# Performance work log

Measured on AMD Instinct MI355X. Metric: run time of the kernel, lower is better.

## Reference

```python
import jax, jax.numpy as jnp
import numpy as np

G = 131072            # number of graphs
NPG = 38              # nodes per graph (from reshape to (*, 38))
N = G * NPG           # total nodes
E = 10 * N            # total edges (avg degree 10)


def leaky_relu(x):
    return jnp.where(x >= 0, x, 0.01 * x)


def setup_inputs() -> dict:
    key = jax.random.key(0)
    ks = jax.random.split(key, 13)
    s = 0.1
    return {
        "x": jax.random.normal(ks[0], (N, 1), jnp.float32),
        "edge_index": jax.random.randint(ks[1], (2, E), 0, N, dtype=jnp.int64)
            if jax.config.read("jax_enable_x64") else jax.random.randint(ks[1], (2, E), 0, N, dtype=jnp.int32),
        "edge_attr": jax.random.normal(ks[2], (E, 1), jnp.float32),
        # NNConv(1,1, Linear(1,1)) params
        "w_edge": jax.random.normal(ks[3], (1, 1), jnp.float32) * s,  # edge MLP weight
        "b_edge": jax.random.normal(ks[4], (1,), jnp.float32) * s,   # edge MLP bias
        "w_root": jax.random.normal(ks[5], (1, 1), jnp.float32) * s, # NNConv root weight
        "b_conv": jax.random.normal(ks[6], (1,), jnp.float32) * s,   # NNConv bias
        # head MLP: 38 -> 4 -> 4 -> 12 (stored as (in, out))
        "W1": jax.random.normal(ks[7], (38, 4), jnp.float32) * s,
        "b1": jax.random.normal(ks[8], (4,), jnp.float32) * s,
        "W2": jax.random.normal(ks[9], (4, 4), jnp.float32) * s,
        "b2": jax.random.normal(ks[10], (4,), jnp.float32) * s,
        "W3": jax.random.normal(ks[11], (4, 12), jnp.float32) * s,
        "b3": jax.random.normal(ks[12], (12,), jnp.float32) * s,
    }


def reference(x, edge_index, edge_attr, w_edge, b_edge, w_root, b_conv,
              W1, b1, W2, b2, W3, b3):
    src, dst = edge_index[0], edge_index[1]
    # per-edge 1x1 transform produced by edge MLP: theta_e = Linear(edge_attr)
    theta = edge_attr @ w_edge + b_edge            # [E, 1]
    # message = x_src * theta (in=out=1 so the matmul is a scalar product)
    msg = x[src] * theta                           # [E, 1] gather + multiply
    agg = jax.ops.segment_sum(msg, dst, num_segments=N)  # scatter-add to targets
    nodes = agg + x @ w_root + b_conv              # [N, 1] add aggr + root + bias
    # dense head over per-graph node vectors (dropout is identity at eval)
    h = nodes.reshape(G, NPG)                      # [G, 38]
    h = leaky_relu(h @ W1 + b1)                    # [G, 4]
    h = leaky_relu(h @ W2 + b2)                    # [G, 4]
    h = leaky_relu(h @ W3 + b3)                    # [G, 12]
    return jax.nn.softmax(h, axis=-1)
```

## Files before the change

### kernel.cpp

```cpp
#include <hip/hip_runtime.h>
#include <hip/hip_fp16.h>

#define NPG 38
#define HEAD_BLK 256
#define SHIFT 14
#define SLICE (1 << SHIFT)
#define DBMAX 320
#define NSB 8
#define NB1 1024
#define P1_THR 512
#define CH 8192
#define P2_THR 512

typedef int      v4i __attribute__((ext_vector_type(4)));
typedef float    v4f __attribute__((ext_vector_type(4)));
typedef unsigned v2u __attribute__((ext_vector_type(2)));

static inline __device__ unsigned short f2h(float f) {
    return __half_as_ushort(__float2half(f));
}
static inline __device__ float h2f(unsigned short b) {
    return __half2float(__ushort_as_half(b));
}

__global__ __launch_bounds__(P1_THR) void k_p1a(
    const int* __restrict__ src, int nquads, int qpb, int sbsz,
    int* __restrict__ histM8)
{
    __shared__ int h8[NSB];
    const int tid = threadIdx.x;
    if (tid < NSB) h8[tid] = 0;
    __syncthreads();
    const int blk = blockIdx.x;
    const int q0 = blk * qpb;
    const int q1 = min(q0 + qpb, nquads);
    const v4i* s4 = (const v4i*)src;
    for (int q = q0 + tid; q < q1; q += P1_THR) {
        v4i s = __builtin_nontemporal_load(s4 + q);
        atomicAdd(&h8[s.x / sbsz], 1);
        atomicAdd(&h8[s.y / sbsz], 1);
        atomicAdd(&h8[s.z / sbsz], 1);
        atomicAdd(&h8[s.w / sbsz], 1);
    }
    __syncthreads();
    if (tid < NSB) histM8[tid * NB1 + blk] = h8[tid];
}

__global__ __launch_bounds__(512) void k_scanM(
    int* __restrict__ histM8, int* __restrict__ sseg)
{
    __shared__ int stot[NSB];
    __shared__ int sbase[NSB + 1];
    const int tid = threadIdx.x;
    const int wid = tid >> 6, lane = tid & 63;

    const int base = wid * NB1 + lane * (NB1 / 64);
    int vals[NB1 / 64];
    int s = 0;
    #pragma unroll
    for (int k = 0; k < NB1 / 64; ++k) { vals[k] = s; s += histM8[base + k]; }
    int excl = s;
    #pragma unroll
    for (int d = 1; d < 64; d <<= 1) {
        int t = __shfl_up(excl, d, 64);
        if (lane >= d) excl += t;
    }
    excl -= s;
    if (lane == 63) stot[wid] = excl + s;
    __syncthreads();
    if (tid == 0) {
        int run = 0;
        for (int i = 0; i < NSB; ++i) { sbase[i] = run; run += stot[i]; }
        sbase[NSB] = run;
    }
    __syncthreads();
    const int b0 = sbase[wid] + excl;
    #pragma unroll
    for (int k = 0; k < NB1 / 64; ++k) histM8[base + k] = vals[k] + b0;
    if (tid < NSB + 1) sseg[tid] = sbase[tid];
}

__global__ __launch_bounds__(P1_THR) void k_p1b(
    const int* __restrict__ src, const int* __restrict__ dst,
    const float* __restrict__ ea,
    const float* __restrict__ w_edge, const float* __restrict__ b_edge,
    int nquads, int qpb, int sbsz,
    const int* __restrict__ histM8,
    v2u* __restrict__ recs)
{
    __shared__ int cur8[NSB];
    const int blk = blockIdx.x;
    if (threadIdx.x < NSB) cur8[threadIdx.x] = histM8[threadIdx.x * NB1 + blk];
    __syncthreads();
    const int q0 = blk * qpb;
    const int q1 = min(q0 + qpb, nquads);
    const float we = w_edge[0], be = b_edge[0];
    const v4i* s4 = (const v4i*)src;
    const v4i* d4 = (const v4i*)dst;
    const v4f* e4 = (const v4f*)ea;
    for (int q = q0 + threadIdx.x; q < q1; q += P1_THR) {
        v4i s = __builtin_nontemporal_load(s4 + q);
        v4i d = __builtin_nontemporal_load(d4 + q);
        v4f e = __builtin_nontemporal_load(e4 + q);
        #pragma unroll
        for (int k = 0; k < 4; ++k) {
            int sv = (k == 0) ? s.x : (k == 1) ? s.y : (k == 2) ? s.z : s.w;
            int dv = (k == 0) ? d.x : (k == 1) ? d.y : (k == 2) ? d.z : d.w;
            float ev = (k == 0) ? e.x : (k == 1) ? e.y : (k == 2) ? e.z : e.w;
            int sb = sv / sbsz;
            int sl = sv - sb * sbsz;
            unsigned short tb = f2h(fmaf(ev, we, be));
            int p = atomicAdd(&cur8[sb], 1);
            v2u r;
            r.x = ((unsigned)(sl & 0xFFFF) << 16) | (unsigned)tb;
            r.y = (unsigned)dv | ((unsigned)(sl >> 16) << 23);
            recs[p] = r;
        }
    }
}

__global__ __launch_bounds__(P2_THR) void k_p2(
    const v2u* __restrict__ recs, const float* __restrict__ x,
    const int* __restrict__ sseg, int sbsz, int DB, int CPS,
    unsigned short* __restrict__ ofsT, unsigned* __restrict__ pairs)
{
    __shared__ __align__(16) unsigned pairbuf[CH];
    __shared__ int hD[DBMAX];
    __shared__ int lofs[DBMAX];
    __shared__ int lcur[DBMAX];

    const int sb = blockIdx.x & 7;
    const int cc = blockIdx.x >> 3;
    const int seg0 = sseg[sb], seg1 = sseg[sb + 1];
    const int start = seg0 + cc * CH;
    if (start >= seg1) return;
    const int n = min(CH, seg1 - start);
    const float* xs = x + (size_t)sb * sbsz;
    const int tid = threadIdx.x;
    const int wid = tid >> 6, lane = tid & 63;

    for (int i = tid; i < DBMAX; i += P2_THR) hD[i] = 0;
    __syncthreads();

    #pragma unroll
    for (int half = 0; half < CH / (8 * P2_THR); ++half) {
        unsigned bk[8];
        #pragma unroll
        for (int k = 0; k < 8; ++k) {
            int idx = tid + (half * 8 + k) * P2_THR;
            bk[k] = (idx < n) ? ((recs[start + idx].y & 0x7FFFFFu) >> SHIFT)
                              : 0xFFFFu;
        }
        #pragma unroll
        for (int k = 0; k < 8; ++k)
            if (bk[k] != 0xFFFFu) atomicAdd(&hD[bk[k]], 1);
    }
    __syncthreads();

    if (wid == 0) {
        const int base = lane * (DBMAX / 64);
        int vals[DBMAX / 64];
        int s = 0;
        #pragma unroll
        for (int k = 0; k < DBMAX / 64; ++k) { vals[k] = s; s += hD[base + k]; }
        int excl = s;
        #pragma unroll
        for (int d = 1; d < 64; d <<= 1) {
            int t = __shfl_up(excl, d, 64);
            if (lane >= d) excl += t;
        }
        excl -= s;
        #pragma unroll
        for (int k = 0; k < DBMAX / 64; ++k) lofs[base + k] = vals[k] + excl;
    }
    __syncthreads();

    const size_t tbase = (size_t)(sb * CPS + cc) * (DBMAX + 1);
    for (int b = tid; b < DB; b += P2_THR) {
        lcur[b] = lofs[b];
        ofsT[tbase + b] = (unsigned short)lofs[b];
    }
    if (tid == 0) ofsT[tbase + DB] = (unsigned short)n;
    __syncthreads();

    #pragma unroll
    for (int half = 0; half < CH / (8 * P2_THR); ++half) {
        v2u r[8];
        #pragma unroll
        for (int k = 0; k < 8; ++k) {
            int idx = tid + (half * 8 + k) * P2_THR;
            if (idx < n) r[k] = recs[start + idx];
            else { r[k].x = 0u; r[k].y = 0u; }
        }
        float xv[8];
        #pragma unroll
        for (int k = 0; k < 8; ++k) {
            int sl = (int)(r[k].x >> 16) | (int)((r[k].y >> 23) << 16);
            xv[k] = xs[sl];
        }
        #pragma unroll
        for (int k = 0; k < 8; ++k) {
            int idx = tid + (half * 8 + k) * P2_THR;
            if (idx < n) {
                unsigned d = r[k].y & 0x7FFFFFu;
                float m = xv[k] * h2f((unsigned short)(r[k].x & 0xFFFFu));
                int li = atomicAdd(&lcur[d >> SHIFT], 1);
                pairbuf[li] = ((d & (SLICE - 1)) << 16) | (unsigned)f2h(m);
            }
        }
    }
    __syncthreads();

    const size_t pbase = (size_t)(sb * CPS + cc) * CH;
    uint4* out4 = reinterpret_cast<uint4*>(pairs + pbase);
    const uint4* pb4 = reinterpret_cast<const uint4*>(pairbuf);
    #pragma unroll
    for (int i = 0; i < CH / 4 / P2_THR; ++i)
        out4[tid + i * P2_THR] = pb4[tid + i * P2_THR];
}

__global__ __launch_bounds__(1024) void k_binB(
    const unsigned* __restrict__ pairs,
    const unsigned short* __restrict__ ofsT,
    const int* __restrict__ sseg, int CPS,
    const float* __restrict__ x,
    const float* __restrict__ w_root, const float* __restrict__ b_conv,
    float* __restrict__ nodes, int N)
{
    __shared__ float slice[SLICE];
    const int b = blockIdx.x;
    for (int i = threadIdx.x; i < SLICE; i += 1024) slice[i] = 0.0f;
    __syncthreads();
    const int wid = threadIdx.x >> 6, lane = threadIdx.x & 63;
    for (int sb = 0; sb < NSB; ++sb) {
        const int len = sseg[sb + 1] - sseg[sb];
        const int ncc = (len + CH - 1) / CH;
        for (int cc = wid; cc < ncc; cc += 16) {
            const int g = sb * CPS + cc;
            const size_t tb = (size_t)g * (DBMAX + 1);
            const int o0 = ofsT[tb + b];
            const int o1 = ofsT[tb + b + 1];
            const unsigned* pc = pairs + (size_t)g * CH;
            for (int j = o0 + lane; j < o1; j += 64) {
                unsigned p = pc[j];
                atomicAdd(&slice[p >> 16], h2f((unsigned short)(p & 0xFFFFu)));
            }
        }
    }
    __syncthreads();
    const float wr = w_root[0], bc = b_conv[0];
    const int gbase = b << SHIFT;
    for (int i = threadIdx.x; i < SLICE; i += 1024) {
        int gi = gbase + i;
        if (gi < N) nodes[gi] = slice[i] + fmaf(__builtin_nontemporal_load(x + gi), wr, bc);
    }
}

__global__ __launch_bounds__(512) void k_count_mid(
    const int* __restrict__ dst, int nquads, int qpb, int DB,
    int* __restrict__ gcntD)
{
    __shared__ int hD[DBMAX];
    for (int i = threadIdx.x; i < DB; i += 512) hD[i] = 0;
    __syncthreads();
    const int q0 = blockIdx.x * qpb;
    const int q1 = min(q0 + qpb, nquads);
    const v4i* d4 = (const v4i*)dst;
    for (int q = q0 + threadIdx.x; q < q1; q += 512) {
        v4i d = __builtin_nontemporal_load(d4 + q);
        atomicAdd(&hD[d.x >> SHIFT], 1);
        atomicAdd(&hD[d.y >> SHIFT], 1);
        atomicAdd(&hD[d.z >> SHIFT], 1);
        atomicAdd(&hD[d.w >> SHIFT], 1);
    }
    __syncthreads();
    for (int i = threadIdx.x; i < DB; i += 512)
        if (hD[i]) atomicAdd(&gcntD[i], hD[i]);
}

__global__ void k_scanD(const int* __restrict__ gcntD, int DB,
                        int* __restrict__ bbaseD, int* __restrict__ gcurD)
{
    if (threadIdx.x == 0 && blockIdx.x == 0) {
        int run = 0;
        for (int i = 0; i < DB; ++i) { bbaseD[i] = run; gcurD[i] = run; run += gcntD[i]; }
        bbaseD[DB] = run;
    }
}

__global__ __launch_bounds__(512) void k_binA_resv(
    const float* __restrict__ x,
    const int* __restrict__ src, const int* __restrict__ dst,
    const float* __restrict__ ea,
    const float* __restrict__ w_edge, const float* __restrict__ b_edge,
    int nquads, int qpb, int DB,
    int* __restrict__ gcurD, unsigned* __restrict__ pairs)
{
    __shared__ int hD[DBMAX];
    __shared__ int cur[DBMAX];
    const int q0 = blockIdx.x * qpb;
    const int q1 = min(q0 + qpb, nquads);
    for (int i = threadIdx.x; i < DB; i += 512) hD[i] = 0;
    __syncthreads();
    const v4i* s4 = (const v4i*)src;
    const v4i* d4 = (const v4i*)dst;
    const v4f* e4 = (const v4f*)ea;
    for (int q = q0 + threadIdx.x; q < q1; q += 512) {
        v4i d = d4[q];
        atomicAdd(&hD[d.x >> SHIFT], 1);
        atomicAdd(&hD[d.y >> SHIFT], 1);
        atomicAdd(&hD[d.z >> SHIFT], 1);
        atomicAdd(&hD[d.w >> SHIFT], 1);
    }
    __syncthreads();
    for (int i = threadIdx.x; i < DB; i += 512) {
        int cnt = hD[i];
        cur[i] = cnt ? atomicAdd(&gcurD[i], cnt) : 0;
    }
    __syncthreads();
    const float we = w_edge[0], be = b_edge[0];
    for (int q = q0 + threadIdx.x; q < q1; q += 512) {
        v4i s = __builtin_nontemporal_load(s4 + q);
        v4i d = d4[q];
        v4f e = __builtin_nontemporal_load(e4 + q);
        #pragma unroll
        for (int k = 0; k < 4; ++k) {
            int sv = (k == 0) ? s.x : (k == 1) ? s.y : (k == 2) ? s.z : s.w;
            unsigned dv = (unsigned)((k == 0) ? d.x : (k == 1) ? d.y : (k == 2) ? d.z : d.w);
            float ev = (k == 0) ? e.x : (k == 1) ? e.y : (k == 2) ? e.z : e.w;
            float m = x[sv] * fmaf(ev, we, be);
            int p = atomicAdd(&cur[dv >> SHIFT], 1);
            pairs[p] = ((dv & (SLICE - 1)) << 16) | (unsigned)f2h(m);
        }
    }
}

__global__ __launch_bounds__(1024) void k_binB_lin(
    const unsigned* __restrict__ pairs,
    const int* __restrict__ bbaseD,
    const float* __restrict__ x,
    const float* __restrict__ w_root, const float* __restrict__ b_conv,
    float* __restrict__ nodes, int N)
{
    __shared__ float slice[SLICE];
    const int b = blockIdx.x;
    for (int i = threadIdx.x; i < SLICE; i += 1024) slice[i] = 0.0f;
    __syncthreads();
    const int p0 = bbaseD[b];
    const int p1 = bbaseD[b + 1];
    for (int i = p0 + threadIdx.x; i < p1; i += 1024) {
        unsigned p = __builtin_nontemporal_load(pairs + i);
        atomicAdd(&slice[p >> 16], h2f((unsigned short)(p & 0xFFFFu)));
    }
    __syncthreads();
    const float wr = w_root[0], bc = b_conv[0];
    const int gbase = b << SHIFT;
    for (int i = threadIdx.x; i < SLICE; i += 1024) {
        int gi = gbase + i;
        if (gi < N) nodes[gi] = slice[i] + fmaf(__builtin_nontemporal_load(x + gi), wr, bc);
    }
}

__global__ __launch_bounds__(256) void edge_kernel_atomic(
    const float* __restrict__ x,
    const int*   __restrict__ src, const int* __restrict__ dst,
    const float* __restrict__ ea,
    const float* __restrict__ w_edge, const float* __restrict__ b_edge,
    float* __restrict__ agg, int E)
{
    const float we = w_edge[0], be = b_edge[0];
    int tid = blockIdx.x * blockDim.x + threadIdx.x;
    int stride = gridDim.x * blockDim.x;
    for (int i = tid; i < E; i += stride)
        atomicAdd(&agg[dst[i]], x[src[i]] * fmaf(ea[i], we, be));
}

__global__ __launch_bounds__(256) void finalize_nodes(
    const float* __restrict__ x, const float* __restrict__ agg,
    const float* __restrict__ w_root, const float* __restrict__ b_conv,
    float* __restrict__ nodes, int N)
{
    const float wr = w_root[0], bc = b_conv[0];
    int i = blockIdx.x * blockDim.x + threadIdx.x;
    int stride = gridDim.x * blockDim.x;
    for (; i < N; i += stride) nodes[i] = agg[i] + fmaf(x[i], wr, bc);
}

__global__ __launch_bounds__(HEAD_BLK) void head_kernel(
    const float* __restrict__ nodes,
    const float* __restrict__ W1, const float* __restrict__ b1,
    const float* __restrict__ W2, const float* __restrict__ b2,
    const float* __restrict__ W3, const float* __restrict__ b3,
    float* __restrict__ out, int G)
{
    __shared__ float s_nodes[HEAD_BLK * NPG];
    __shared__ float s_W1[NPG * 4];
    __shared__ float s_W2[4 * 4];
    __shared__ float s_W3[4 * 12];
    __shared__ float s_b1[4];
    __shared__ float s_b2[4];
    __shared__ float s_b3[12];

    const int tid = threadIdx.x;
    if (tid < NPG * 4) s_W1[tid] = W1[tid];
    if (tid >= 160 && tid < 176) s_W2[tid - 160] = W2[tid - 160];
    if (tid >= 176 && tid < 224) s_W3[tid - 176] = W3[tid - 176];
    if (tid >= 224 && tid < 228) s_b1[tid - 224] = b1[tid - 224];
    if (tid >= 228 && tid < 232) s_b2[tid - 228] = b2[tid - 228];
    if (tid >= 232 && tid < 244) s_b3[tid - 232] = b3[tid - 232];

    const int g0 = blockIdx.x * HEAD_BLK;
    const size_t ebase = (size_t)g0 * NPG;
    const int nelem = HEAD_BLK * NPG;
    const int avail = min(nelem, (G - g0) * NPG);
    for (int i = tid; i < avail; i += HEAD_BLK) s_nodes[i] = nodes[ebase + i];
    __syncthreads();

    const int g = g0 + tid;
    if (g >= G) return;
    const float* nd = &s_nodes[tid * NPG];

    float h1[4];
    #pragma unroll
    for (int k = 0; k < 4; ++k) h1[k] = s_b1[k];
    #pragma unroll
    for (int j = 0; j < NPG; ++j) {
        const float nj = nd[j];
        #pragma unroll
        for (int k = 0; k < 4; ++k) h1[k] = fmaf(nj, s_W1[j * 4 + k], h1[k]);
    }
    #pragma unroll
    for (int k = 0; k < 4; ++k) h1[k] = h1[k] >= 0.0f ? h1[k] : 0.01f * h1[k];

    float h2[4];
    #pragma unroll
    for (int k = 0; k < 4; ++k) {
        float a = s_b2[k];
        #pragma unroll
        for (int j = 0; j < 4; ++j) a = fmaf(h1[j], s_W2[j * 4 + k], a);
        h2[k] = a >= 0.0f ? a : 0.01f * a;
    }

    float h3[12];
    #pragma unroll
    for (int k = 0; k < 12; ++k) {
        float a = s_b3[k];
        #pragma unroll
        for (int j = 0; j < 4; ++j) a = fmaf(h2[j], s_W3[j * 12 + k], a);
        h3[k] = a >= 0.0f ? a : 0.01f * a;
    }

    float m = h3[0];
    #pragma unroll
    for (int k = 1; k < 12; ++k) m = fmaxf(m, h3[k]);
    float sum = 0.0f;
    #pragma unroll
    for (int k = 0; k < 12; ++k) { h3[k] = expf(h3[k] - m); sum += h3[k]; }
    const float inv = 1.0f / sum;

    float4* o = reinterpret_cast<float4*>(out + (size_t)g * 12);
    o[0] = make_float4(h3[0] * inv, h3[1] * inv, h3[2]  * inv, h3[3]  * inv);
    o[1] = make_float4(h3[4] * inv, h3[5] * inv, h3[6]  * inv, h3[7]  * inv);
    o[2] = make_float4(h3[8] * inv, h3[9] * inv, h3[10] * inv, h3[11] * inv);
}

extern "C" void kernel_launch(void* const* d_in, const int* in_sizes, int n_in,
                              void* d_out, int out_size, void* d_ws, size_t ws_size,
                              hipStream_t stream)
{
    const float* x      = (const float*)d_in[0];
    const int*   eidx   = (const int*)  d_in[1];
    const float* ea     = (const float*)d_in[2];
    const float* w_edge = (const float*)d_in[3];
    const float* b_edge = (const float*)d_in[4];
    const float* w_root = (const float*)d_in[5];
    const float* b_conv = (const float*)d_in[6];
    const float* W1 = (const float*)d_in[7];
    const float* b1 = (const float*)d_in[8];
    const float* W2 = (const float*)d_in[9];
    const float* b2 = (const float*)d_in[10];
    const float* W3 = (const float*)d_in[11];
    const float* b3 = (const float*)d_in[12];
    float* out = (float*)d_out;

    const int N = in_sizes[0];
    const int E = in_sizes[2];
    const int G = N / NPG;
    const int* src = eidx;
    const int* dst = eidx + E;
    const int nquads = E / 4;
    const int DB = (N + SLICE - 1) >> SHIFT;

    const int hblocks = (G + HEAD_BLK - 1) / HEAD_BLK;
    char* ws = (char*)d_ws;

    const bool quadok = (E % 4) == 0 && DB <= DBMAX && DB >= 1;
    const int  sbsz   = (N % NSB == 0) ? (N / NSB) : 0;

    const int CPS = ((E + NSB - 1) / NSB + 32768 + CH - 1) / CH;
    const size_t NCHG = (size_t)NSB * CPS;

    const size_t META_INTS = (size_t)NSB * NB1 + (NSB + 1) + DBMAX + DBMAX + (DBMAX + 1);

    size_t off_pairs = (size_t)E * 8;
    size_t sz_pairs  = NCHG * CH * 4;
    size_t off_ofsT  = off_pairs + sz_pairs;
    size_t sz_ofsT   = (NCHG * (DBMAX + 1) * 2 + 15) & ~(size_t)15;
    size_t off_nodes = off_ofsT + sz_ofsT;
    size_t off_meta  = off_nodes + (size_t)N * 4;
    size_t need_v4   = off_meta + META_INTS * 4;

    size_t off_nodes_mid = (size_t)E * 4;
    size_t off_meta_mid  = off_nodes_mid + (size_t)N * 4;
    size_t need_mid      = off_meta_mid + META_INTS * 4;

    if (quadok && sbsz > 0 && need_v4 <= ws_size) {
        v2u*            recs  = (v2u*)ws;
        unsigned*       pairs = (unsigned*)(ws + off_pairs);
        unsigned short* ofsT  = (unsigned short*)(ws + off_ofsT);
        float*          nodes = (float*)(ws + off_nodes);
        int*            meta  = (int*)(ws + off_meta);
        int* histM8 = meta;
        int* sseg   = meta + NSB * NB1;

        const int qpb = (nquads + NB1 - 1) / NB1;
        k_p1a<<<NB1, P1_THR, 0, stream>>>(src, nquads, qpb, sbsz, histM8);
        k_scanM<<<1, 512, 0, stream>>>(histM8, sseg);
        k_p1b<<<NB1, P1_THR, 0, stream>>>(src, dst, ea, w_edge, b_edge,
                                          nquads, qpb, sbsz, histM8, recs);
        k_p2<<<NSB * CPS, P2_THR, 0, stream>>>(recs, x, sseg, sbsz, DB, CPS,
                                               ofsT, pairs);
        k_binB<<<DB, 1024, 0, stream>>>(pairs, ofsT, sseg, CPS, x,
                                        w_root, b_conv, nodes, N);
        head_kernel<<<hblocks, HEAD_BLK, 0, stream>>>(nodes, W1, b1, W2, b2,
                                                      W3, b3, out, G);
    } else if (quadok && need_mid <= ws_size) {
        unsigned* pairs = (unsigned*)ws;
        float*    nodes = (float*)(ws + off_nodes_mid);
        int*      meta  = (int*)(ws + off_meta_mid);
        int* gcntD  = meta + NSB * NB1 + (NSB + 1);
        int* gcurD  = gcntD + DBMAX;
        int* bbaseD = gcurD + DBMAX;

        hipMemsetAsync(gcntD, 0, DBMAX * sizeof(int), stream);
        const int NBm = 2048;
        const int qpbm = (nquads + NBm - 1) / NBm;
        k_count_mid<<<NBm, 512, 0, stream>>>(dst, nquads, qpbm, DB, gcntD);
        k_scanD<<<1, 64, 0, stream>>>(gcntD, DB, bbaseD, gcurD);
        k_binA_resv<<<NBm, 512, 0, stream>>>(x, src, dst, ea, w_edge, b_edge,
                                             nquads, qpbm, DB, gcurD, pairs);
        k_binB_lin<<<DB, 1024, 0, stream>>>(pairs, bbaseD, x, w_root, b_conv,
                                            nodes, N);
        head_kernel<<<hblocks, HEAD_BLK, 0, stream>>>(nodes, W1, b1, W2, b2,
                                                      W3, b3, out, G);
    } else {
        float* agg   = (float*)d_ws;
        float* nodes = agg + N;
        hipMemsetAsync(agg, 0, (size_t)N * sizeof(float), stream);
        edge_kernel_atomic<<<2048, 256, 0, stream>>>(x, src, dst, ea, w_edge,
                                                     b_edge, agg, E);
        finalize_nodes<<<2048, 256, 0, stream>>>(x, agg, w_root, b_conv, nodes, N);
        head_kernel<<<hblocks, HEAD_BLK, 0, stream>>>(nodes, W1, b1, W2, b2,
                                                      W3, b3, out, G);
    }
}
```

Measured before the change: 1.172 ms.

## Halve dst slice size and load-balance binB via prefix-scan over flat chunks

Destination slices shrink from 16K to 8K nodes, doubling the number of binB blocks for better occupancy and a smaller LDS footprint. Chunks in k_p2 now tile the edge array flatly, ignoring src-bucket boundaries, and recover each record's src bucket by comparing its position against the segment offsets. k_binB no longer assigns one wave per chunk. It prefix-sums per-chunk counts in phases of 1024 chunks and distributes the pairs evenly across all threads with a binary search. This removes wave-level imbalance and padding waste, at the cost of per-element binary searches and more ofsT reads.

```diff
diff --git a/kernel.cpp b/kernel.cpp
--- a/kernel.cpp
+++ b/kernel.cpp
@@ -3,14 +3,16 @@
 
 #define NPG 38
 #define HEAD_BLK 256
-#define SHIFT 14
+#define SHIFT 13
 #define SLICE (1 << SHIFT)
-#define DBMAX 320
+#define DBMAX 640
 #define NSB 8
 #define NB1 1024
 #define P1_THR 512
 #define CH 8192
 #define P2_THR 512
+#define BB_THR 1024
+#define BB_PH 1024
 
 typedef int      v4i __attribute__((ext_vector_type(4)));
 typedef float    v4f __attribute__((ext_vector_type(4)));
@@ -121,24 +123,24 @@
 
 __global__ __launch_bounds__(P2_THR) void k_p2(
     const v2u* __restrict__ recs, const float* __restrict__ x,
-    const int* __restrict__ sseg, int sbsz, int DB, int CPS,
+    const int* __restrict__ sseg, int sbsz, int DB, int NCH, int bpx, int E,
     unsigned short* __restrict__ ofsT, unsigned* __restrict__ pairs)
 {
     __shared__ __align__(16) unsigned pairbuf[CH];
     __shared__ int hD[DBMAX];
     __shared__ int lofs[DBMAX];
     __shared__ int lcur[DBMAX];
-
-    const int sb = blockIdx.x & 7;
-    const int cc = blockIdx.x >> 3;
-    const int seg0 = sseg[sb], seg1 = sseg[sb + 1];
-    const int start = seg0 + cc * CH;
-    if (start >= seg1) return;
-    const int n = min(CH, seg1 - start);
-    const float* xs = x + (size_t)sb * sbsz;
+    __shared__ int sS[NSB + 1];
+
+    const int jraw = blockIdx.x;
+    const int j = (jraw & 7) * bpx + (jraw >> 3);
+    if (j >= NCH) return;
+    const int start = j * CH;
+    const int n = min(CH, E - start);
     const int tid = threadIdx.x;
     const int wid = tid >> 6, lane = tid & 63;
 
+    if (tid < NSB + 1) sS[tid] = sseg[tid];
     for (int i = tid; i < DBMAX; i += P2_THR) hD[i] = 0;
     __syncthreads();
 
@@ -175,7 +177,7 @@
     }
     __syncthreads();
 
-    const size_t tbase = (size_t)(sb * CPS + cc) * (DBMAX + 1);
+    const size_t tbase = (size_t)j * (DBMAX + 1);
     for (int b = tid; b < DB; b += P2_THR) {
         lcur[b] = lofs[b];
         ofsT[tbase + b] = (unsigned short)lofs[b];
@@ -195,8 +197,13 @@
         float xv[8];
         #pragma unroll
         for (int k = 0; k < 8; ++k) {
+            int idx = tid + (half * 8 + k) * P2_THR;
+            int gp = start + min(idx, n - 1);
+            int sbr = 0;
+            #pragma unroll
+            for (int s = 1; s < NSB; ++s) sbr += (gp >= sS[s]);
             int sl = (int)(r[k].x >> 16) | (int)((r[k].y >> 23) << 16);
-            xv[k] = xs[sl];
+            xv[k] = x[(size_t)sbr * sbsz + sl];
         }
         #pragma unroll
         for (int k = 0; k < 8; ++k) {
@@ -211,7 +218,7 @@
     }
     __syncthreads();
 
-    const size_t pbase = (size_t)(sb * CPS + cc) * CH;
+    const size_t pbase = (size_t)j * CH;
     uint4* out4 = reinterpret_cast<uint4*>(pairs + pbase);
     const uint4* pb4 = reinterpret_cast<const uint4*>(pairbuf);
     #pragma unroll
@@ -219,38 +226,77 @@
         out4[tid + i * P2_THR] = pb4[tid + i * P2_THR];
 }
 
-__global__ __launch_bounds__(1024) void k_binB(
+__global__ __launch_bounds__(BB_THR) void k_binB(
     const unsigned* __restrict__ pairs,
     const unsigned short* __restrict__ ofsT,
-    const int* __restrict__ sseg, int CPS,
+    int NCH, int DB,
     const float* __restrict__ x,
     const float* __restrict__ w_root, const float* __restrict__ b_conv,
     float* __restrict__ nodes, int N)
 {
     __shared__ float slice[SLICE];
+    __shared__ unsigned short so0[BB_PH];
+    __shared__ int spre[BB_PH];
+    __shared__ int sTot;
     const int b = blockIdx.x;
-    for (int i = threadIdx.x; i < SLICE; i += 1024) slice[i] = 0.0f;
-    __syncthreads();
-    const int wid = threadIdx.x >> 6, lane = threadIdx.x & 63;
-    for (int sb = 0; sb < NSB; ++sb) {
-        const int len = sseg[sb + 1] - sseg[sb];
-        const int ncc = (len + CH - 1) / CH;
-        for (int cc = wid; cc < ncc; cc += 16) {
-            const int g = sb * CPS + cc;
-            const size_t tb = (size_t)g * (DBMAX + 1);
-            const int o0 = ofsT[tb + b];
-            const int o1 = ofsT[tb + b + 1];
-            const unsigned* pc = pairs + (size_t)g * CH;
-            for (int j = o0 + lane; j < o1; j += 64) {
-                unsigned p = pc[j];
-                atomicAdd(&slice[p >> 16], h2f((unsigned short)(p & 0xFFFFu)));
+    const int tid = threadIdx.x;
+    const int wid = tid >> 6, lane = tid & 63;
+
+    for (int i = tid; i < SLICE; i += BB_THR) slice[i] = 0.0f;
+    __syncthreads();
+
+    for (int ch0 = 0; ch0 < NCH; ch0 += BB_PH) {
+        const int nc = min(BB_PH, NCH - ch0);
+        for (int c = tid; c < nc; c += BB_THR) {
+            const size_t tb = (size_t)(ch0 + c) * (DBMAX + 1);
+            int o0 = ofsT[tb + b];
+            int o1 = ofsT[tb + b + 1];
+            so0[c] = (unsigned short)o0;
+            spre[c] = o1 - o0;
+        }
+        __syncthreads();
+        if (wid == 0) {
+            const int base = lane * (BB_PH / 64);
+            int vals[BB_PH / 64];
+            int s = 0;
+            #pragma unroll
+            for (int k = 0; k < BB_PH / 64; ++k) {
+                int idx = base + k;
+                int t = (idx < nc) ? spre[idx] : 0;
+                vals[k] = s; s += t;
             }
-        }
-    }
-    __syncthreads();
+            int excl = s;
+            #pragma unroll
+            for (int d = 1; d < 64; d <<= 1) {
+                int t = __shfl_up(excl, d, 64);
+                if (lane >= d) excl += t;
+            }
+            excl -= s;
+            #pragma unroll
+            for (int k = 0; k < BB_PH / 64; ++k) {
+                int idx = base + k;
+                if (idx < nc) spre[idx] = vals[k] + excl;
+            }
+            if (lane == 63) sTot = excl + s;
+        }
+        __syncthreads();
+        const int total = sTot;
+        for (int i = tid; i < total; i += BB_THR) {
+            int lo = 0, hi = nc - 1;
+            while (lo < hi) {
+                int mid = (lo + hi + 1) >> 1;
+                if (spre[mid] <= i) lo = mid; else hi = mid - 1;
+            }
+            int off = i - spre[lo];
+            unsigned p = pairs[(size_t)(ch0 + lo) * CH + so0[lo] + off];
+            atomicAdd(&slice[p >> 16], h2f((unsigned short)(p & 0xFFFFu)));
+        }
+        __syncthreads();
+    }
+
     const float wr = w_root[0], bc = b_conv[0];
     const int gbase = b << SHIFT;
-    for (int i = threadIdx.x; i < SLICE; i += 1024) {
+    for (int i = tid; i < SLICE; i += BB_THR) {
         int gi = gbase + i;
         if (gi < N) nodes[gi] = slice[i] + fmaf(__builtin_nontemporal_load(x + gi), wr, bc);
     }
@@ -497,24 +543,24 @@
     const bool quadok = (E % 4) == 0 && DB <= DBMAX && DB >= 1;
     const int  sbsz   = (N % NSB == 0) ? (N / NSB) : 0;
 
-    const int CPS = ((E + NSB - 1) / NSB + 32768 + CH - 1) / CH;
-    const size_t NCHG = (size_t)NSB * CPS;
+    const int NCH = (E + CH - 1) / CH;
+    const int bpx = (NCH + 7) / 8;
 
     const size_t META_INTS = (size_t)NSB * NB1 + (NSB + 1) + DBMAX + DBMAX + (DBMAX + 1);
 
     size_t off_pairs = (size_t)E * 8;
-    size_t sz_pairs  = NCHG * CH * 4;
+    size_t sz_pairs  = (size_t)NCH * CH * 4;
     size_t off_ofsT  = off_pairs + sz_pairs;
-    size_t sz_ofsT   = (NCHG * (DBMAX + 1) * 2 + 15) & ~(size_t)15;
+    size_t sz_ofsT   = ((size_t)NCH * (DBMAX + 1) * 2 + 15) & ~(size_t)15;
     size_t off_nodes = off_ofsT + sz_ofsT;
     size_t off_meta  = off_nodes + (size_t)N * 4;
-    size_t need_v4   = off_meta + META_INTS * 4;
+    size_t need_v5   = off_meta + META_INTS * 4;
 
     size_t off_nodes_mid = (size_t)E * 4;
     size_t off_meta_mid  = off_nodes_mid + (size_t)N * 4;
     size_t need_mid      = off_meta_mid + META_INTS * 4;
 
-    if (quadok && sbsz > 0 && need_v4 <= ws_size) {
+    if (quadok && sbsz > 0 && need_v5 <= ws_size) {
         v2u*            recs  = (v2u*)ws;
         unsigned*       pairs = (unsigned*)(ws + off_pairs);
         unsigned short* ofsT  = (unsigned short*)(ws + off_ofsT);
@@ -528,10 +574,10 @@
         k_scanM<<<1, 512, 0, stream>>>(histM8, sseg);
         k_p1b<<<NB1, P1_THR, 0, stream>>>(src, dst, ea, w_edge, b_edge,
                                           nquads, qpb, sbsz, histM8, recs);
-        k_p2<<<NSB * CPS, P2_THR, 0, stream>>>(recs, x, sseg, sbsz, DB, CPS,
-                                               ofsT, pairs);
-        k_binB<<<DB, 1024, 0, stream>>>(pairs, ofsT, sseg, CPS, x,
-                                        w_root, b_conv, nodes, N);
+        k_p2<<<8 * bpx, P2_THR, 0, stream>>>(recs, x, sseg, sbsz, DB, NCH, bpx,
+                                             E, ofsT, pairs);
+        k_binB<<<DB, BB_THR, 0, stream>>>(pairs, ofsT, NCH, DB, x,
+                                          w_root, b_conv, nodes, N);
         head_kernel<<<hblocks, HEAD_BLK, 0, stream>>>(nodes, W1, b1, W2, b2,
                                                       W3, b3, out, G);
     } else if (quadok && need_mid <= ws_size) {
```

Measured after the change: 1.099 ms. -6.2%, faster.
